# Kernel tuning notes

Measured on AMD Instinct MI355X. Metric: run time of the kernel, lower is better.

## Reference

```python
import jax, jax.numpy as jnp
import numpy as np

KM_ITERS = 20  # fixed Lloyd iterations (scipy kmeans iterates to tolerance with random init;
               # we use deterministic min/max init so centroid 0 = dark, 1 = bright)


def _kmeans_mask(img2d):
    """2-means clustering of pixel intensities of one [H,W] image + border-vote flip."""
    H, W = img2d.shape
    x = img2d.reshape(-1)  # [N]
    c0 = jnp.stack([x.min(), x.max()])  # deterministic init: centroid0=min, centroid1=max

    def step(c, _):
        code = jnp.argmin(jnp.abs(x[:, None] - c[None, :]), axis=1)  # [N] in {0,1}
        one = code == 1
        n1 = jnp.sum(one)
        n0 = x.shape[0] - n1
        s1 = jnp.sum(jnp.where(one, x, jnp.zeros_like(x)))
        s0 = jnp.sum(x) - s1
        c_new = jnp.stack([s0 / jnp.maximum(n0, 1).astype(x.dtype),
                           s1 / jnp.maximum(n1, 1).astype(x.dtype)])
        return c_new, None

    c, _ = jax.lax.scan(step, c0, None, length=KM_ITERS)
    # final assignment (scipy vq step)
    code = jnp.argmin(jnp.abs(x[:, None] - c[None, :]), axis=1).reshape(H, W)

    # border vote: if >=3 borders are mostly cluster-1, flip so text region is 1
    fc = code[:, 0].sum()
    lc = code[:, -1].sum()
    fr = code[0, :].sum()
    lr = code[-1, :].sum()
    num = ((fr > W // 2).astype(jnp.int32) + (lr > W // 2).astype(jnp.int32)
           + (fc > H // 2).astype(jnp.int32) + (lc > H // 2).astype(jnp.int32))
    mask = jnp.where(num >= 3, 1 - code, code)
    return mask.astype(img2d.dtype)


def get_mask(img_tensor):
    gray = img_tensor.mean(axis=1)  # [B,H,W]
    # clustering is non-differentiable in the original (runs on detached CPU numpy)
    masks = jax.vmap(_kmeans_mask)(jax.lax.stop_gradient(gray))
    return masks[:, None, :, :]  # [B,1,H,W]


def setup_inputs() -> dict:
    key = jax.random.key(0)
    k1, k2 = jax.random.split(key)
    B, C, H, W = 128, 3, 256, 256
    hr_img = jax.random.uniform(k1, (B, C, H, W), dtype=jnp.float32)
    sr_mask = jax.random.uniform(k2, (B, 1, H, W), dtype=jnp.float32)
    return {"hr_img": hr_img, "sr_mask": sr_mask}


def reference(hr_img, sr_mask):
    hr_mask = get_mask(hr_img)  # same spatial size -> no interpolation branch
    return jnp.mean((sr_mask - hr_mask) ** 2)
```

## Files before the change

kernel.cpp:

```cpp
#include <hip/hip_runtime.h>


constexpr int NB   = 2048;
constexpr int NPIX = 65536;
constexpr int KM_ITERS = 20;
constexpr float QINV  = 1.0f / 65536.0f;
constexpr float BINW  = 1.0f / 2048.0f;

constexpr size_t OFF_MINENC = 0;
constexpr size_t OFF_MAXU   = 512;
constexpr size_t OFF_TINFO  = 1024;
constexpr size_t OFF_BORD   = 3072;
constexpr size_t OFF_HCNT   = 8192;
constexpr size_t OFF_GRAY   = OFF_HCNT + (size_t)128 * NB * 4;
constexpr size_t OFF_BSUM   = OFF_GRAY + (size_t)128 * NPIX * 2;
constexpr size_t MEMSET_BYTES = OFF_GRAY;

__device__ __forceinline__ float waveSumF(float v) {
#pragma unroll
    for (int off = 32; off > 0; off >>= 1) v += __shfl_down(v, off, 64);
    return v;
}
__device__ __forceinline__ unsigned waveMinU(unsigned v) {
#pragma unroll
    for (int off = 32; off > 0; off >>= 1) v = min(v, (unsigned)__shfl_down((int)v, off, 64));
    return v;
}
__device__ __forceinline__ unsigned waveMaxU(unsigned v) {
#pragma unroll
    for (int off = 32; off > 0; off >>= 1) v = max(v, (unsigned)__shfl_down((int)v, off, 64));
    return v;
}

__global__ __launch_bounds__(256) void kA_hist(
        const float* __restrict__ hr, unsigned* __restrict__ minenc,
        unsigned* __restrict__ maxu, unsigned* __restrict__ hcnt,
        ushort* __restrict__ gray) {
    const int img = blockIdx.x >> 3, part = blockIdx.x & 7, tid = threadIdx.x;
    const int lane = tid & 63, wid = tid >> 6;

    __shared__ unsigned hcL[NB];
    __shared__ unsigned smn[4], smx[4];
    for (int j = tid; j < NB; j += 256) hcL[j] = 0u;
    __syncthreads();

    const float* r = hr + (size_t)img * 3 * NPIX;
    const float* g = r + NPIX;
    const float* b = g + NPIX;
    ushort* gp = gray + (size_t)img * NPIX;

    unsigned umn = 65535u, umx = 0u;
#pragma unroll
    for (int i = 0; i < 8; ++i) {
        const int p = part * 8192 + i * 1024 + tid * 4;
        float4 rr = *(const float4*)(r + p);
        float4 gg = *(const float4*)(g + p);
        float4 bb = *(const float4*)(b + p);
        float x[4] = { (rr.x + gg.x + bb.x) * (1.0f / 3.0f),
                       (rr.y + gg.y + bb.y) * (1.0f / 3.0f),
                       (rr.z + gg.z + bb.z) * (1.0f / 3.0f),
                       (rr.w + gg.w + bb.w) * (1.0f / 3.0f) };
        unsigned u[4];
#pragma unroll
        for (int j = 0; j < 4; ++j) {
            unsigned uu = (unsigned)(x[j] * 65536.0f);
            uu = min(uu, 65535u);
            u[j] = uu;
            umn = min(umn, uu); umx = max(umx, uu);
            atomicAdd(&hcL[uu >> 5], 1u);
        }
        ushort4 u4;
        u4.x = (ushort)u[0]; u4.y = (ushort)u[1];
        u4.z = (ushort)u[2]; u4.w = (ushort)u[3];
        *(ushort4*)(gp + p) = u4;
    }
    __syncthreads();

    for (int j = tid; j < NB; j += 256) {
        const unsigned c = hcL[j];
        if (c) atomicAdd(&hcnt[(size_t)img * NB + j], c);
    }

    umn = waveMinU(umn); umx = waveMaxU(umx);
    if (lane == 0) { smn[wid] = umn; smx[wid] = umx; }
    __syncthreads();
    if (tid == 0) {
        const unsigned bmn = min(min(smn[0], smn[1]), min(smn[2], smn[3]));
        const unsigned bmx = max(max(smx[0], smx[1]), max(smx[2], smx[3]));
        atomicMax(&maxu[img], bmx);
        atomicMax(&minenc[img], 65535u - bmn);
    }
}

__global__ __launch_bounds__(256) void kB_lloyd(
        const unsigned* __restrict__ minenc, const unsigned* __restrict__ maxu,
        const unsigned* __restrict__ hcnt, float4* __restrict__ tinfo) {
    const int img = blockIdx.x, tid = threadIdx.x;
    __shared__ float sN[NB + 1], sS[NB + 1];
    __shared__ float tN[256], tS[256];

    const int base = tid * 8;
    float n8[8], s8[8];
#pragma unroll
    for (int u = 0; u < 8; ++u) {
        const float c = (float)hcnt[(size_t)img * NB + base + u];
        n8[u] = c;
        s8[u] = c * (((float)(base + u) + 0.484375f) * BINW);
    }
    float accN = 0.0f, accS = 0.0f;
#pragma unroll
    for (int u = 7; u >= 0; --u) {
        accN += n8[u]; n8[u] = accN;
        accS += s8[u]; s8[u] = accS;
    }
    tN[tid] = accN; tS[tid] = accS;
    __syncthreads();
    for (int off = 1; off < 256; off <<= 1) {
        float aN = 0.0f, aS = 0.0f;
        if (tid + off < 256) { aN = tN[tid + off]; aS = tS[tid + off]; }
        __syncthreads();
        tN[tid] += aN; tS[tid] += aS;
        __syncthreads();
    }
    const float exN = (tid < 255) ? tN[tid + 1] : 0.0f;
    const float exS = (tid < 255) ? tS[tid + 1] : 0.0f;
#pragma unroll
    for (int u = 0; u < 8; ++u) { sN[base + u] = n8[u] + exN; sS[base + u] = s8[u] + exS; }
    if (tid == 0) { sN[NB] = 0.0f; sS[NB] = 0.0f; }
    __syncthreads();

    if (tid == 0) {
        float c0 = (float)(65535u - minenc[img]) * QINV;
        float c1 = (float)maxu[img] * QINV;
        const float Stot = sS[0];
        const float Ntot = (float)NPIX;
#pragma unroll 1
        for (int it = 0; it < KM_ITERS; ++it) {
            const float t = 0.5f * (c0 + c1);
            float n1, s1;
            if (c1 == c0) { n1 = 0.0f; s1 = 0.0f; }
            else {
                const float f = t * (float)NB;
                int k = (int)floorf(f);
                k = max(0, min(NB - 1, k));
                float frac = (float)(k + 1) - f;
                frac = fminf(fmaxf(frac, 0.0f), 1.0f);
                const float cntk = sN[k] - sN[k + 1];
                const float aN = sN[k + 1] + cntk * frac;
                const float aS = sS[k + 1] +
                                 cntk * frac * 0.5f * (t + (float)(k + 1) * BINW);
                if (c1 > c0) { n1 = aN; s1 = aS; }
                else         { n1 = Ntot - aN; s1 = Stot - aS; }
            }
            const float c1n = s1 / fmaxf(n1, 1.0f);
            const float c0n = (Stot - s1) / fmaxf(Ntot - n1, 1.0f);
            if (c1n == c1 && c0n == c0) break;
            c0 = c0n; c1 = c1n;
        }
        float tf, hii;
        if (c1 == c0) { tf = -1e30f; hii = 0.0f; }
        else { tf = 0.5f * (c0 + c1); hii = (c1 > c0) ? 1.0f : 0.0f; }
        tinfo[img] = make_float4(tf, hii, 0.0f, 0.0f);
    }
}

__global__ __launch_bounds__(256) void kC_mse(
        const ushort* __restrict__ gray, const float* __restrict__ sr,
        const float4* __restrict__ tinfo, unsigned* __restrict__ bord,
        float2* __restrict__ bsum) {
    const int img = blockIdx.x >> 3, part = blockIdx.x & 7, tid = threadIdx.x;
    const int lane = tid & 63, wid = tid >> 6;
    __shared__ float sA0[4], sA1[4];
    __shared__ float4 sB[4];

    const float4 ti = tinfo[img];
    const float t = ti.x;
    const bool hi = (ti.y != 0.0f);

    const ushort* gp = gray + (size_t)img * NPIX;
    const float*  sp = sr   + (size_t)img * NPIX;

    float a0 = 0.0f, a1 = 0.0f;
    float fr = 0.0f, lr = 0.0f, fc = 0.0f, lc = 0.0f;
#pragma unroll
    for (int i = 0; i < 8; ++i) {
        const int p = part * 8192 + i * 1024 + tid * 4;
        ushort4 u4 = *(const ushort4*)(gp + p);
        float4  ss = *(const float4*)(sp + p);
        const unsigned uu[4] = { u4.x, u4.y, u4.z, u4.w };
        const float    sv[4] = { ss.x, ss.y, ss.z, ss.w };
        const int row = p >> 8;
#pragma unroll
        for (int j = 0; j < 4; ++j) {
            const float x = (float)uu[j] * QINV;
            const bool one = hi ? (x > t) : (x < t);
            const float m = one ? 1.0f : 0.0f;
            const float d0 = sv[j] - m;
            const float d1 = sv[j] - (1.0f - m);
            a0 += d0 * d0;
            a1 += d1 * d1;
            const int col = (p & 255) + j;
            if (col == 0)   fc += m;
            if (col == 255) lc += m;
            if (row == 0)   fr += m;
            if (row == 255) lr += m;
        }
    }
    a0 = waveSumF(a0); a1 = waveSumF(a1);
    fr = waveSumF(fr); lr = waveSumF(lr); fc = waveSumF(fc); lc = waveSumF(lc);
    if (lane == 0) { sA0[wid] = a0; sA1[wid] = a1; sB[wid] = make_float4(fr, lr, fc, lc); }
    __syncthreads();
    if (tid == 0) {
        bsum[blockIdx.x] = make_float2(sA0[0] + sA0[1] + sA0[2] + sA0[3],
                                       sA1[0] + sA1[1] + sA1[2] + sA1[3]);
        const float FR = sB[0].x + sB[1].x + sB[2].x + sB[3].x;
        const float LR = sB[0].y + sB[1].y + sB[2].y + sB[3].y;
        const float FC = sB[0].z + sB[1].z + sB[2].z + sB[3].z;
        const float LC = sB[0].w + sB[1].w + sB[2].w + sB[3].w;
        unsigned* bb = bord + (size_t)img * 4;
        if (FR > 0.5f) atomicAdd(&bb[0], (unsigned)(FR + 0.5f));
        if (LR > 0.5f) atomicAdd(&bb[1], (unsigned)(LR + 0.5f));
        if (FC > 0.5f) atomicAdd(&bb[2], (unsigned)(FC + 0.5f));
        if (LC > 0.5f) atomicAdd(&bb[3], (unsigned)(LC + 0.5f));
    }
}

__global__ __launch_bounds__(256) void kD_final(
        const unsigned* __restrict__ bord, const float2* __restrict__ bsum,
        float* __restrict__ out) {
    const int tid = threadIdx.x, lane = tid & 63, wid = tid >> 6;
    __shared__ float flipS[128];
    __shared__ float sm[4];
    if (tid < 128) {
        const unsigned* bb = bord + (size_t)tid * 4;
        const int num = (bb[0] > 128u) + (bb[1] > 128u) + (bb[2] > 128u) + (bb[3] > 128u);
        flipS[tid] = (num >= 3) ? 1.0f : 0.0f;
    }
    __syncthreads();
    float acc = 0.0f;
#pragma unroll
    for (int q = 0; q < 4; ++q) {
        const int e = tid * 4 + q;
        const float2 v = bsum[e];
        acc += (flipS[e >> 3] != 0.0f) ? v.y : v.x;
    }
    acc = waveSumF(acc);
    if (lane == 0) sm[wid] = acc;
    __syncthreads();
    if (tid == 0) out[0] = (sm[0] + sm[1] + sm[2] + sm[3]) * (1.0f / 8388608.0f);
}

extern "C" void kernel_launch(void* const* d_in, const int* in_sizes, int n_in,
                              void* d_out, int out_size, void* d_ws, size_t ws_size,
                              hipStream_t stream) {
    const float* hr = (const float*)d_in[0];
    const float* sr = (const float*)d_in[1];
    float* out = (float*)d_out;

    char* ws = (char*)d_ws;
    unsigned* minenc = (unsigned*)(ws + OFF_MINENC);
    unsigned* maxu   = (unsigned*)(ws + OFF_MAXU);
    float4*   tinfo  = (float4*)(ws + OFF_TINFO);
    unsigned* bord   = (unsigned*)(ws + OFF_BORD);
    unsigned* hcnt   = (unsigned*)(ws + OFF_HCNT);
    ushort*   gray   = (ushort*)(ws + OFF_GRAY);
    float2*   bsum   = (float2*)(ws + OFF_BSUM);

    hipMemsetAsync(d_ws, 0, MEMSET_BYTES, stream);
    kA_hist <<<1024, 256, 0, stream>>>(hr, minenc, maxu, hcnt, gray);
    kB_lloyd<<< 128, 256, 0, stream>>>(minenc, maxu, hcnt, tinfo);
    kC_mse  <<<1024, 256, 0, stream>>>(gray, sr, tinfo, bord, bsum);
    kD_final<<<   1, 256, 0, stream>>>(bord, bsum, out);
}
```

Before: 187.9 us.

## Compute MSE from per-bin sr sums, dropping the gray buffer and second pass

The first kernel now also reads sr and builds, for each intensity bin, the sum of sr values, plus a per-block sum of sr squared. It writes per-block histogram slabs instead of using global atomics. The MSE for both mask polarities is then derived algebraically from prefix sums at the threshold bin, so the full-resolution gray image and the second full pass over sr are no longer needed. Only border pixels are stored for the vote, and a last-block atomic counter replaces the final kernel and the memset. The cost is float atomicAdd into shared memory in the hot loop, and the MSE for pixels in the threshold bin is interpolated rather than exact, so results can differ slightly.

```diff
diff --git a/kernel.cpp b/kernel.cpp
--- a/kernel.cpp
+++ b/kernel.cpp
@@ -4,17 +4,16 @@
 constexpr int NB   = 2048;
 constexpr int NPIX = 65536;
 constexpr int KM_ITERS = 20;
-constexpr float QINV  = 1.0f / 65536.0f;
-constexpr float BINW  = 1.0f / 2048.0f;
-
-constexpr size_t OFF_MINENC = 0;
-constexpr size_t OFF_MAXU   = 512;
-constexpr size_t OFF_TINFO  = 1024;
-constexpr size_t OFF_BORD   = 3072;
-constexpr size_t OFF_HCNT   = 8192;
-constexpr size_t OFF_GRAY   = OFF_HCNT + (size_t)128 * NB * 4;
-constexpr size_t OFF_BSUM   = OFF_GRAY + (size_t)128 * NPIX * 2;
-constexpr size_t MEMSET_BYTES = OFF_GRAY;
+constexpr float QINV = 1.0f / 65536.0f;
+constexpr float BINW = 1.0f / 2048.0f;
+
+constexpr size_t OFF_MMN = 0;
+constexpr size_t OFF_MMX = 4096;
+constexpr size_t OFF_SR2 = 8192;
+constexpr size_t OFF_ACC = 12288;
+constexpr size_t OFF_BG  = 16384;
+constexpr size_t OFF_CNT = OFF_BG + 262144;
+constexpr size_t OFF_SV  = OFF_CNT + 8388608;
 
 __device__ __forceinline__ float waveSumF(float v) {
 #pragma unroll
@@ -33,33 +32,42 @@
 }
 
 __global__ __launch_bounds__(256) void kA_hist(
-        const float* __restrict__ hr, unsigned* __restrict__ minenc,
-        unsigned* __restrict__ maxu, unsigned* __restrict__ hcnt,
-        ushort* __restrict__ gray) {
-    const int img = blockIdx.x >> 3, part = blockIdx.x & 7, tid = threadIdx.x;
-    const int lane = tid & 63, wid = tid >> 6;
-
-    __shared__ unsigned hcL[NB];
+        const float* __restrict__ hr, const float* __restrict__ sr,
+        unsigned* __restrict__ mmn, unsigned* __restrict__ mmx,
+        float* __restrict__ bsr2, ushort* __restrict__ bg,
+        unsigned* __restrict__ cslab, float* __restrict__ vslab,
+        float* __restrict__ acc, unsigned* __restrict__ done) {
+    const int blk = blockIdx.x, img = blk >> 3, part = blk & 7;
+    const int tid = threadIdx.x, lane = tid & 63, wid = tid >> 6;
+
+    __shared__ unsigned hc[NB];
+    __shared__ float    hv[NB];
     __shared__ unsigned smn[4], smx[4];
-    for (int j = tid; j < NB; j += 256) hcL[j] = 0u;
-    __syncthreads();
-
-    const float* r = hr + (size_t)img * 3 * NPIX;
-    const float* g = r + NPIX;
-    const float* b = g + NPIX;
-    ushort* gp = gray + (size_t)img * NPIX;
+    __shared__ float    ssq[4];
+    for (int j = tid; j < NB; j += 256) { hc[j] = 0u; hv[j] = 0.0f; }
+    if (blk == 0 && tid == 0) { *acc = 0.0f; *done = 0u; }
+    __syncthreads();
+
+    const float* rr = hr + (size_t)img * 3 * NPIX;
+    const float* gg = rr + NPIX;
+    const float* bb = gg + NPIX;
+    const float* sp = sr + (size_t)img * NPIX;
+    ushort* bgp = bg + (size_t)img * 1024;
 
     unsigned umn = 65535u, umx = 0u;
+    float sq = 0.0f;
 #pragma unroll
     for (int i = 0; i < 8; ++i) {
         const int p = part * 8192 + i * 1024 + tid * 4;
-        float4 rr = *(const float4*)(r + p);
-        float4 gg = *(const float4*)(g + p);
-        float4 bb = *(const float4*)(b + p);
-        float x[4] = { (rr.x + gg.x + bb.x) * (1.0f / 3.0f),
-                       (rr.y + gg.y + bb.y) * (1.0f / 3.0f),
-                       (rr.z + gg.z + bb.z) * (1.0f / 3.0f),
-                       (rr.w + gg.w + bb.w) * (1.0f / 3.0f) };
+        float4 r4 = *(const float4*)(rr + p);
+        float4 g4 = *(const float4*)(gg + p);
+        float4 b4 = *(const float4*)(bb + p);
+        float4 s4 = *(const float4*)(sp + p);
+        const float x[4] = { (r4.x + g4.x + b4.x) * (1.0f / 3.0f),
+                             (r4.y + g4.y + b4.y) * (1.0f / 3.0f),
+                             (r4.z + g4.z + b4.z) * (1.0f / 3.0f),
+                             (r4.w + g4.w + b4.w) * (1.0f / 3.0f) };
+        const float sv[4] = { s4.x, s4.y, s4.z, s4.w };
         unsigned u[4];
 #pragma unroll
         for (int j = 0; j < 4; ++j) {
@@ -67,71 +75,116 @@
             uu = min(uu, 65535u);
             u[j] = uu;
             umn = min(umn, uu); umx = max(umx, uu);
-            atomicAdd(&hcL[uu >> 5], 1u);
-        }
-        ushort4 u4;
-        u4.x = (ushort)u[0]; u4.y = (ushort)u[1];
-        u4.z = (ushort)u[2]; u4.w = (ushort)u[3];
-        *(ushort4*)(gp + p) = u4;
+            atomicAdd(&hc[uu >> 5], 1u);
+            atomicAdd(&hv[uu >> 5], sv[j]);
+            sq += sv[j] * sv[j];
+        }
+        const int row = p >> 8, colb = p & 255;
+        if (row == 0) {
+            ushort4 q; q.x = (ushort)u[0]; q.y = (ushort)u[1];
+            q.z = (ushort)u[2]; q.w = (ushort)u[3];
+            *(ushort4*)(bgp + colb) = q;
+        }
+        if (row == 255) {
+            ushort4 q; q.x = (ushort)u[0]; q.y = (ushort)u[1];
+            q.z = (ushort)u[2]; q.w = (ushort)u[3];
+            *(ushort4*)(bgp + 256 + colb) = q;
+        }
+        if (colb == 0)   bgp[512 + row] = (ushort)u[0];
+        if (colb == 252) bgp[768 + row] = (ushort)u[3];
     }
     __syncthreads();
 
     for (int j = tid; j < NB; j += 256) {
-        const unsigned c = hcL[j];
-        if (c) atomicAdd(&hcnt[(size_t)img * NB + j], c);
-    }
-
-    umn = waveMinU(umn); umx = waveMaxU(umx);
-    if (lane == 0) { smn[wid] = umn; smx[wid] = umx; }
+        cslab[(size_t)blk * NB + j] = hc[j];
+        vslab[(size_t)blk * NB + j] = hv[j];
+    }
+
+    sq = waveSumF(sq); umn = waveMinU(umn); umx = waveMaxU(umx);
+    if (lane == 0) { ssq[wid] = sq; smn[wid] = umn; smx[wid] = umx; }
     __syncthreads();
     if (tid == 0) {
-        const unsigned bmn = min(min(smn[0], smn[1]), min(smn[2], smn[3]));
-        const unsigned bmx = max(max(smx[0], smx[1]), max(smx[2], smx[3]));
-        atomicMax(&maxu[img], bmx);
-        atomicMax(&minenc[img], 65535u - bmn);
-    }
-}
-
-__global__ __launch_bounds__(256) void kB_lloyd(
-        const unsigned* __restrict__ minenc, const unsigned* __restrict__ maxu,
-        const unsigned* __restrict__ hcnt, float4* __restrict__ tinfo) {
+        bsr2[blk] = ssq[0] + ssq[1] + ssq[2] + ssq[3];
+        mmn[blk] = min(min(smn[0], smn[1]), min(smn[2], smn[3]));
+        mmx[blk] = max(max(smx[0], smx[1]), max(smx[2], smx[3]));
+    }
+}
+
+__global__ __launch_bounds__(256) void kB_all(
+        const unsigned* __restrict__ mmn, const unsigned* __restrict__ mmx,
+        const float* __restrict__ bsr2, const ushort* __restrict__ bg,
+        const unsigned* __restrict__ cslab, const float* __restrict__ vslab,
+        float* __restrict__ acc, unsigned* __restrict__ done,
+        float* __restrict__ out) {
     const int img = blockIdx.x, tid = threadIdx.x;
-    __shared__ float sN[NB + 1], sS[NB + 1];
-    __shared__ float tN[256], tS[256];
+    const int lane = tid & 63, wid = tid >> 6;
+    __shared__ float sN[NB + 1], sS[NB + 1], sV[NB + 1];
+    __shared__ float tN[256], tS[256], tV[256];
+    __shared__ float bres[4];
+    __shared__ float4 sB4[4];
 
     const int base = tid * 8;
-    float n8[8], s8[8];
+    unsigned aC[8] = {0u,0u,0u,0u,0u,0u,0u,0u};
+    float    aV[8] = {0.f,0.f,0.f,0.f,0.f,0.f,0.f,0.f};
+#pragma unroll
+    for (int s = 0; s < 8; ++s) {
+        const unsigned* cp = cslab + (size_t)(img * 8 + s) * NB + base;
+        const float*    vp = vslab + (size_t)(img * 8 + s) * NB + base;
+        const uint4  c0 = *(const uint4*)cp;
+        const uint4  c1 = *(const uint4*)(cp + 4);
+        const float4 v0 = *(const float4*)vp;
+        const float4 v1 = *(const float4*)(vp + 4);
+        aC[0] += c0.x; aC[1] += c0.y; aC[2] += c0.z; aC[3] += c0.w;
+        aC[4] += c1.x; aC[5] += c1.y; aC[6] += c1.z; aC[7] += c1.w;
+        aV[0] += v0.x; aV[1] += v0.y; aV[2] += v0.z; aV[3] += v0.w;
+        aV[4] += v1.x; aV[5] += v1.y; aV[6] += v1.z; aV[7] += v1.w;
+    }
+
+    float n8[8], s8[8], v8[8];
 #pragma unroll
     for (int u = 0; u < 8; ++u) {
-        const float c = (float)hcnt[(size_t)img * NB + base + u];
+        const float c = (float)aC[u];
         n8[u] = c;
         s8[u] = c * (((float)(base + u) + 0.484375f) * BINW);
-    }
-    float accN = 0.0f, accS = 0.0f;
+        v8[u] = aV[u];
+    }
+    float accN = 0.0f, accS = 0.0f, accV = 0.0f;
 #pragma unroll
     for (int u = 7; u >= 0; --u) {
         accN += n8[u]; n8[u] = accN;
         accS += s8[u]; s8[u] = accS;
-    }
-    tN[tid] = accN; tS[tid] = accS;
+        accV += v8[u]; v8[u] = accV;
+    }
+    tN[tid] = accN; tS[tid] = accS; tV[tid] = accV;
     __syncthreads();
     for (int off = 1; off < 256; off <<= 1) {
-        float aN = 0.0f, aS = 0.0f;
-        if (tid + off < 256) { aN = tN[tid + off]; aS = tS[tid + off]; }
+        float aNN = 0.0f, aSS = 0.0f, aVV = 0.0f;
+        if (tid + off < 256) { aNN = tN[tid + off]; aSS = tS[tid + off]; aVV = tV[tid + off]; }
         __syncthreads();
-        tN[tid] += aN; tS[tid] += aS;
+        tN[tid] += aNN; tS[tid] += aSS; tV[tid] += aVV;
         __syncthreads();
     }
     const float exN = (tid < 255) ? tN[tid + 1] : 0.0f;
     const float exS = (tid < 255) ? tS[tid + 1] : 0.0f;
-#pragma unroll
-    for (int u = 0; u < 8; ++u) { sN[base + u] = n8[u] + exN; sS[base + u] = s8[u] + exS; }
-    if (tid == 0) { sN[NB] = 0.0f; sS[NB] = 0.0f; }
+    const float exV = (tid < 255) ? tV[tid + 1] : 0.0f;
+#pragma unroll
+    for (int u = 0; u < 8; ++u) {
+        sN[base + u] = n8[u] + exN;
+        sS[base + u] = s8[u] + exS;
+        sV[base + u] = v8[u] + exV;
+    }
+    if (tid == 0) { sN[NB] = 0.0f; sS[NB] = 0.0f; sV[NB] = 0.0f; }
     __syncthreads();
 
     if (tid == 0) {
-        float c0 = (float)(65535u - minenc[img]) * QINV;
-        float c1 = (float)maxu[img] * QINV;
+        unsigned bmn = 65535u, bmx = 0u;
+#pragma unroll
+        for (int s = 0; s < 8; ++s) {
+            bmn = min(bmn, mmn[img * 8 + s]);
+            bmx = max(bmx, mmx[img * 8 + s]);
+        }
+        float c0 = (float)bmn * QINV;
+        float c1 = (float)bmx * QINV;
         const float Stot = sS[0];
         const float Ntot = (float)NPIX;
 #pragma unroll 1
@@ -146,108 +199,74 @@
                 float frac = (float)(k + 1) - f;
                 frac = fminf(fmaxf(frac, 0.0f), 1.0f);
                 const float cntk = sN[k] - sN[k + 1];
-                const float aN = sN[k + 1] + cntk * frac;
-                const float aS = sS[k + 1] +
-                                 cntk * frac * 0.5f * (t + (float)(k + 1) * BINW);
-                if (c1 > c0) { n1 = aN; s1 = aS; }
-                else         { n1 = Ntot - aN; s1 = Stot - aS; }
+                const float aNt = sN[k + 1] + cntk * frac;
+                const float aSt = sS[k + 1] +
+                                  cntk * frac * 0.5f * (t + (float)(k + 1) * BINW);
+                if (c1 > c0) { n1 = aNt; s1 = aSt; }
+                else         { n1 = Ntot - aNt; s1 = Stot - aSt; }
             }
             const float c1n = s1 / fmaxf(n1, 1.0f);
             const float c0n = (Stot - s1) / fmaxf(Ntot - n1, 1.0f);
             if (c1n == c1 && c0n == c0) break;
             c0 = c0n; c1 = c1n;
         }
-        float tf, hii;
-        if (c1 == c0) { tf = -1e30f; hii = 0.0f; }
-        else { tf = 0.5f * (c0 + c1); hii = (c1 > c0) ? 1.0f : 0.0f; }
-        tinfo[img] = make_float4(tf, hii, 0.0f, 0.0f);
-    }
-}
-
-__global__ __launch_bounds__(256) void kC_mse(
-        const ushort* __restrict__ gray, const float* __restrict__ sr,
-        const float4* __restrict__ tinfo, unsigned* __restrict__ bord,
-        float2* __restrict__ bsum) {
-    const int img = blockIdx.x >> 3, part = blockIdx.x & 7, tid = threadIdx.x;
-    const int lane = tid & 63, wid = tid >> 6;
-    __shared__ float sA0[4], sA1[4];
-    __shared__ float4 sB[4];
-
-    const float4 ti = tinfo[img];
-    const float t = ti.x;
-    const bool hi = (ti.y != 0.0f);
-
-    const ushort* gp = gray + (size_t)img * NPIX;
-    const float*  sp = sr   + (size_t)img * NPIX;
-
-    float a0 = 0.0f, a1 = 0.0f;
-    float fr = 0.0f, lr = 0.0f, fc = 0.0f, lc = 0.0f;
-#pragma unroll
-    for (int i = 0; i < 8; ++i) {
-        const int p = part * 8192 + i * 1024 + tid * 4;
-        ushort4 u4 = *(const ushort4*)(gp + p);
-        float4  ss = *(const float4*)(sp + p);
-        const unsigned uu[4] = { u4.x, u4.y, u4.z, u4.w };
-        const float    sv[4] = { ss.x, ss.y, ss.z, ss.w };
-        const int row = p >> 8;
-#pragma unroll
-        for (int j = 0; j < 4; ++j) {
-            const float x = (float)uu[j] * QINV;
-            const bool one = hi ? (x > t) : (x < t);
-            const float m = one ? 1.0f : 0.0f;
-            const float d0 = sv[j] - m;
-            const float d1 = sv[j] - (1.0f - m);
-            a0 += d0 * d0;
-            a1 += d1 * d1;
-            const int col = (p & 255) + j;
-            if (col == 0)   fc += m;
-            if (col == 255) lc += m;
-            if (row == 0)   fr += m;
-            if (row == 255) lr += m;
-        }
-    }
-    a0 = waveSumF(a0); a1 = waveSumF(a1);
+
+        float Sr2 = 0.0f;
+#pragma unroll
+        for (int s = 0; s < 8; ++s) Sr2 += bsr2[img * 8 + s];
+        const float SvTot = sV[0];
+
+        float tf, hii, n1, s1v;
+        if (c1 == c0) { tf = -1e30f; hii = 0.0f; n1 = 0.0f; s1v = 0.0f; }
+        else {
+            tf = 0.5f * (c0 + c1);
+            const float f = tf * (float)NB;
+            int k = (int)floorf(f);
+            k = max(0, min(NB - 1, k));
+            float frac = (float)(k + 1) - f;
+            frac = fminf(fmaxf(frac, 0.0f), 1.0f);
+            const float cntk = sN[k] - sN[k + 1];
+            const float aNt = sN[k + 1] + cntk * frac;
+            const float svk = sV[k] - sV[k + 1];
+            const float aSv = sV[k + 1] + svk * frac;
+            if (c1 > c0) { hii = 1.0f; n1 = aNt;        s1v = aSv; }
+            else         { hii = 0.0f; n1 = Ntot - aNt; s1v = SvTot - aSv; }
+        }
+        bres[0] = tf; bres[1] = hii;
+        bres[2] = Sr2 - 2.0f * s1v + n1;
+        bres[3] = Sr2 - 2.0f * (SvTot - s1v) + (Ntot - n1);
+    }
+    __syncthreads();
+
+    const float tf = bres[0];
+    const bool hi = (bres[1] != 0.0f);
+    const ushort* bp = bg + (size_t)img * 1024;
+    const float x0 = (float)bp[tid]       * QINV;
+    const float x1 = (float)bp[256 + tid] * QINV;
+    const float x2 = (float)bp[512 + tid] * QINV;
+    const float x3 = (float)bp[768 + tid] * QINV;
+    float fr = (hi ? (x0 > tf) : (x0 < tf)) ? 1.0f : 0.0f;
+    float lr = (hi ? (x1 > tf) : (x1 < tf)) ? 1.0f : 0.0f;
+    float fc = (hi ? (x2 > tf) : (x2 < tf)) ? 1.0f : 0.0f;
+    float lc = (hi ? (x3 > tf) : (x3 < tf)) ? 1.0f : 0.0f;
     fr = waveSumF(fr); lr = waveSumF(lr); fc = waveSumF(fc); lc = waveSumF(lc);
-    if (lane == 0) { sA0[wid] = a0; sA1[wid] = a1; sB[wid] = make_float4(fr, lr, fc, lc); }
+    if (lane == 0) sB4[wid] = make_float4(fr, lr, fc, lc);
     __syncthreads();
     if (tid == 0) {
-        bsum[blockIdx.x] = make_float2(sA0[0] + sA0[1] + sA0[2] + sA0[3],
-                                       sA1[0] + sA1[1] + sA1[2] + sA1[3]);
-        const float FR = sB[0].x + sB[1].x + sB[2].x + sB[3].x;
-        const float LR = sB[0].y + sB[1].y + sB[2].y + sB[3].y;
-        const float FC = sB[0].z + sB[1].z + sB[2].z + sB[3].z;
-        const float LC = sB[0].w + sB[1].w + sB[2].w + sB[3].w;
-        unsigned* bb = bord + (size_t)img * 4;
-        if (FR > 0.5f) atomicAdd(&bb[0], (unsigned)(FR + 0.5f));
-        if (LR > 0.5f) atomicAdd(&bb[1], (unsigned)(LR + 0.5f));
-        if (FC > 0.5f) atomicAdd(&bb[2], (unsigned)(FC + 0.5f));
-        if (LC > 0.5f) atomicAdd(&bb[3], (unsigned)(LC + 0.5f));
-    }
-}
-
-__global__ __launch_bounds__(256) void kD_final(
-        const unsigned* __restrict__ bord, const float2* __restrict__ bsum,
-        float* __restrict__ out) {
-    const int tid = threadIdx.x, lane = tid & 63, wid = tid >> 6;
-    __shared__ float flipS[128];
-    __shared__ float sm[4];
-    if (tid < 128) {
-        const unsigned* bb = bord + (size_t)tid * 4;
-        const int num = (bb[0] > 128u) + (bb[1] > 128u) + (bb[2] > 128u) + (bb[3] > 128u);
-        flipS[tid] = (num >= 3) ? 1.0f : 0.0f;
-    }
-    __syncthreads();
-    float acc = 0.0f;
-#pragma unroll
-    for (int q = 0; q < 4; ++q) {
-        const int e = tid * 4 + q;
-        const float2 v = bsum[e];
-        acc += (flipS[e >> 3] != 0.0f) ? v.y : v.x;
-    }
-    acc = waveSumF(acc);
-    if (lane == 0) sm[wid] = acc;
-    __syncthreads();
-    if (tid == 0) out[0] = (sm[0] + sm[1] + sm[2] + sm[3]) * (1.0f / 8388608.0f);
+        const float FR = sB4[0].x + sB4[1].x + sB4[2].x + sB4[3].x;
+        const float LR = sB4[0].y + sB4[1].y + sB4[2].y + sB4[3].y;
+        const float FC = sB4[0].z + sB4[1].z + sB4[2].z + sB4[3].z;
+        const float LC = sB4[0].w + sB4[1].w + sB4[2].w + sB4[3].w;
+        const int num = (FR > 128.0f) + (LR > 128.0f) + (FC > 128.0f) + (LC > 128.0f);
+        const float chosen = (num >= 3) ? bres[3] : bres[2];
+        atomicAdd(acc, chosen);
+        __threadfence();
+        const unsigned old = atomicAdd(done, 1u);
+        if (old == 127u) {
+            const float tot = atomicAdd(acc, 0.0f);
+            out[0] = tot * (1.0f / 8388608.0f);
+        }
+    }
 }
 
 extern "C" void kernel_launch(void* const* d_in, const int* in_sizes, int n_in,
@@ -258,17 +277,15 @@
     float* out = (float*)d_out;
 
     char* ws = (char*)d_ws;
-    unsigned* minenc = (unsigned*)(ws + OFF_MINENC);
-    unsigned* maxu   = (unsigned*)(ws + OFF_MAXU);
-    float4*   tinfo  = (float4*)(ws + OFF_TINFO);
-    unsigned* bord   = (unsigned*)(ws + OFF_BORD);
-    unsigned* hcnt   = (unsigned*)(ws + OFF_HCNT);
-    ushort*   gray   = (ushort*)(ws + OFF_GRAY);
-    float2*   bsum   = (float2*)(ws + OFF_BSUM);
-
-    hipMemsetAsync(d_ws, 0, MEMSET_BYTES, stream);
-    kA_hist <<<1024, 256, 0, stream>>>(hr, minenc, maxu, hcnt, gray);
-    kB_lloyd<<< 128, 256, 0, stream>>>(minenc, maxu, hcnt, tinfo);
-    kC_mse  <<<1024, 256, 0, stream>>>(gray, sr, tinfo, bord, bsum);
-    kD_final<<<   1, 256, 0, stream>>>(bord, bsum, out);
-}
+    unsigned* mmn   = (unsigned*)(ws + OFF_MMN);
+    unsigned* mmx   = (unsigned*)(ws + OFF_MMX);
+    float*    bsr2  = (float*)(ws + OFF_SR2);
+    float*    acc   = (float*)(ws + OFF_ACC);
+    unsigned* done  = (unsigned*)(ws + OFF_ACC + 4);
+    ushort*   bg    = (ushort*)(ws + OFF_BG);
+    unsigned* cslab = (unsigned*)(ws + OFF_CNT);
+    float*    vslab = (float*)(ws + OFF_SV);
+
+    kA_hist<<<1024, 256, 0, stream>>>(hr, sr, mmn, mmx, bsr2, bg, cslab, vslab, acc, done);
+    kB_all <<< 128, 256, 0, stream>>>(mmn, mmx, bsr2, bg, cslab, vslab, acc, done, out);
+}
```

New measurement: 189.1 us. About the same (+0.6%).
